# Performance work log

Measured on AMD Instinct MI355X. Metric: run time of the kernel, lower is better.

The kernel has to match this reference:

```python
import jax, jax.numpy as jnp
import numpy as np

EPS = 0.0  # init eps

def setup_inputs() -> dict:
    key = jax.random.key(0)
    k1, k2, k3 = jax.random.split(key, 3)
    n_nodes = 100000
    n_edges = 6400000
    edge_weight = jax.random.uniform(k1, (n_edges,), dtype=jnp.float32)  # non-negative, required by norm='both'
    src = jax.random.randint(k2, (n_edges,), 0, n_nodes, dtype=jnp.int32)
    dst = jax.random.randint(k3, (n_edges,), 0, n_nodes, dtype=jnp.int32)
    return {"edge_weight": edge_weight, "src": src, "dst": dst, "num_nodes": n_nodes}

def reference(edge_weight, src, dst, num_nodes):
    # norm='both': out-degree (weighted) per source node via reversed graph,
    # in-degree (weighted) per destination node; both as segment sums over edges.
    out_deg = jax.ops.segment_sum(edge_weight, src, num_segments=num_nodes) + EPS
    in_deg = jax.ops.segment_sum(edge_weight, dst, num_segments=num_nodes) + EPS
    src_norm = out_deg ** -0.5  # [N]
    dst_norm = in_deg ** -0.5   # [N]
    # gather per-edge norms and multiply with edge weight
    return src_norm[src] * dst_norm[dst] * edge_weight
```

## Files before the change

### kernel.cpp

```cpp
#include <hip/hip_runtime.h>
#include <hip/hip_fp16.h>


#define N_NODES 100000
#define TWO_N   (2 * N_NODES)
#define THREADS 1024
#define GBLK    1024
#define KMAX    4
#define SCALE_F   512.0f
#define INV_SCALE 0.001953125f

__global__ __launch_bounds__(THREADS, 4)
void hist_kernel(const float4* __restrict__ w4,
                 const int4* __restrict__ src4,
                 const int4* __restrict__ dst4,
                 const float* __restrict__ w,
                 const int* __restrict__ src,
                 const int* __restrict__ dst,
                 unsigned* __restrict__ parts,
                 int n4, int n_edges, int P, int C, int bins, int chunk4,
                 int swz)
{
    extern __shared__ unsigned lds[];
    int j, c;
    if (swz) {
        const int x = blockIdx.x & 7;
        const int r = blockIdx.x >> 3;
        j = r % P;
        c = x + 8 * (r / P);
    } else {
        j = blockIdx.x / C;
        c = blockIdx.x - j * C;
    }
    const int lo = j * bins;

    for (int k = threadIdx.x; k < bins; k += THREADS) lds[k] = 0;
    __syncthreads();

    const int beg = c * chunk4;
    const int end = min(n4, beg + chunk4);
    const int t   = threadIdx.x;

#define QUAD(wv, sv, dv)                                                      \
    do {                                                                      \
        unsigned v0 = (unsigned)((wv).x * SCALE_F + 0.5f);                    \
        unsigned v1 = (unsigned)((wv).y * SCALE_F + 0.5f);                    \
        unsigned v2 = (unsigned)((wv).z * SCALE_F + 0.5f);                    \
        unsigned v3 = (unsigned)((wv).w * SCALE_F + 0.5f);                    \
        int a0 = (sv).x - lo, a1 = (sv).y - lo, a2 = (sv).z - lo, a3 = (sv).w - lo; \
        int b0 = (dv).x - lo, b1 = (dv).y - lo, b2 = (dv).z - lo, b3 = (dv).w - lo; \
        if ((unsigned)a0 < (unsigned)bins) atomicAdd(&lds[a0], v0);           \
        if ((unsigned)a1 < (unsigned)bins) atomicAdd(&lds[a1], v1);           \
        if ((unsigned)a2 < (unsigned)bins) atomicAdd(&lds[a2], v2);           \
        if ((unsigned)a3 < (unsigned)bins) atomicAdd(&lds[a3], v3);           \
        if ((unsigned)b0 < (unsigned)bins) atomicAdd(&lds[b0], v0 << 16);     \
        if ((unsigned)b1 < (unsigned)bins) atomicAdd(&lds[b1], v1 << 16);     \
        if ((unsigned)b2 < (unsigned)bins) atomicAdd(&lds[b2], v2 << 16);     \
        if ((unsigned)b3 < (unsigned)bins) atomicAdd(&lds[b3], v3 << 16);     \
    } while (0)

    {
        const int total = end - beg;
        const int trips = (total + 2 * THREADS - 1) / (2 * THREADS);
        int i = beg + t;

        float4 wc0, wc1, wn0, wn1;
        int4   sc0, sc1, sn0, sn1, dc0, dc1, dn0, dn1;
        bool   pc0, pc1, pn0, pn1;

        pn0 = i < end;
        pn1 = (i + THREADS) < end;
        if (pn0) { wn0 = w4[i];           sn0 = src4[i];           dn0 = dst4[i]; }
        if (pn1) { wn1 = w4[i + THREADS]; sn1 = src4[i + THREADS]; dn1 = dst4[i + THREADS]; }

        for (int tr = 0; tr < trips; ++tr) {
            wc0 = wn0; sc0 = sn0; dc0 = dn0; pc0 = pn0;
            wc1 = wn1; sc1 = sn1; dc1 = dn1; pc1 = pn1;

            const int ni = i + 2 * THREADS;
            pn0 = (tr + 1 < trips) && (ni < end);
            pn1 = (tr + 1 < trips) && ((ni + THREADS) < end);
            if (pn0) { wn0 = w4[ni];           sn0 = src4[ni];           dn0 = dst4[ni]; }
            if (pn1) { wn1 = w4[ni + THREADS]; sn1 = src4[ni + THREADS]; dn1 = dst4[ni + THREADS]; }

            __builtin_amdgcn_sched_barrier(0);

            if (pc0) QUAD(wc0, sc0, dc0);
            if (pc1) QUAD(wc1, sc1, dc1);
            i = ni;
        }
    }
#undef QUAD

    if (c == C - 1 && threadIdx.x == 0) {
        for (int e = n4 * 4; e < n_edges; ++e) {
            unsigned v = (unsigned)(w[e] * SCALE_F + 0.5f);
            int a = src[e] - lo;
            int b = dst[e] - lo;
            if ((unsigned)a < (unsigned)bins) atomicAdd(&lds[a], v);
            if ((unsigned)b < (unsigned)bins) atomicAdd(&lds[b], v << 16);
        }
    }

    __syncthreads();
    unsigned* op = parts + ((size_t)j * C + c) * bins;
    for (int k = threadIdx.x; k < bins; k += THREADS)
        __builtin_nontemporal_store(lds[k], op + k);
}

__global__ void reduce_rsqrt_kernel(const unsigned* __restrict__ parts,
                                    __half* __restrict__ normh,
                                    int P, int C, int bins)
{
    int i = blockIdx.x * blockDim.x + threadIdx.x;
    if (i >= N_NODES) return;
    int p = i / bins;
    int b = i - p * bins;
    const unsigned* base = parts + ((size_t)p * C) * bins + b;
    unsigned lo0 = 0, hi0 = 0, lo1 = 0, hi1 = 0, lo2 = 0, hi2 = 0, lo3 = 0, hi3 = 0;
    int c = 0;
    for (; c + 3 < C; c += 4) {
        unsigned v0 = base[(size_t)(c + 0) * bins];
        unsigned v1 = base[(size_t)(c + 1) * bins];
        unsigned v2 = base[(size_t)(c + 2) * bins];
        unsigned v3 = base[(size_t)(c + 3) * bins];
        lo0 += v0 & 0xFFFFu; hi0 += v0 >> 16;
        lo1 += v1 & 0xFFFFu; hi1 += v1 >> 16;
        lo2 += v2 & 0xFFFFu; hi2 += v2 >> 16;
        lo3 += v3 & 0xFFFFu; hi3 += v3 >> 16;
    }
    for (; c < C; ++c) {
        unsigned v = base[(size_t)c * bins];
        lo0 += v & 0xFFFFu; hi0 += v >> 16;
    }
    unsigned lo_s = lo0 + lo1 + lo2 + lo3;
    unsigned hi_s = hi0 + hi1 + hi2 + hi3;
    normh[i]           = __float2half(1.0f / sqrtf((float)lo_s * INV_SCALE));
    normh[N_NODES + i] = __float2half(1.0f / sqrtf((float)hi_s * INV_SCALE));
}

__global__ void degree_atomic_kernel(const float* __restrict__ w,
                                     const int* __restrict__ src,
                                     const int* __restrict__ dst,
                                     float* __restrict__ deg,
                                     int n_edges)
{
    int i = blockIdx.x * blockDim.x + threadIdx.x;
    int stride = gridDim.x * blockDim.x;
    for (; i < n_edges; i += stride) {
        float wi = w[i];
        atomicAdd(&deg[src[i]], wi);
        atomicAdd(&deg[N_NODES + dst[i]], wi);
    }
}

__global__ void rsqrt_half_kernel(const float* __restrict__ deg,
                                  __half* __restrict__ normh, int n)
{
    int i = blockIdx.x * blockDim.x + threadIdx.x;
    if (i < n) normh[i] = __float2half(1.0f / sqrtf(deg[i]));
}

__global__ __launch_bounds__(GBLK, 8)
void prod_kernel(const float4* __restrict__ w4,
                 const int4* __restrict__ src4,
                 const int4* __restrict__ dst4,
                 const __half* __restrict__ srcn_h,
                 const __half* __restrict__ dstn_h,
                 float4* __restrict__ out4,
                 int n4, int n_edges, int qpb, int NR,
                 const float* __restrict__ w,
                 const int* __restrict__ src,
                 const int* __restrict__ dst,
                 float* __restrict__ out)
{
    extern __shared__ __half lh[];
    const int q0   = blockIdx.x * qpb;
    const int qend = min(n4, q0 + qpb);
    const int t    = threadIdx.x;
    const int passes  = (N_NODES + NR - 1) / NR;
    const int half_u4 = NR >> 3;
    const int tot_u4  = NR >> 2;

    float4 pr[KMAX];
    int4   sv[KMAX], dv[KMAX];
    bool   val[KMAX];
#pragma unroll
    for (int k = 0; k < KMAX; ++k) {
        const int q = q0 + k * GBLK + t;
        val[k] = q < qend;
        if (val[k]) {
            pr[k] = w4[q];
            sv[k] = src4[q];
            dv[k] = dst4[q];
        }
    }

    for (int p = 0; p < passes; ++p) {
        if (p > 0) __syncthreads();
        {
            const int base_ = p * NR;
            const uint4* gs = (const uint4*)(srcn_h + base_);
            const uint4* gd = (const uint4*)(dstn_h + base_);
            uint4* lb = (uint4*)lh;
            for (int idx = t; idx < tot_u4; idx += GBLK)
                lb[idx] = (idx < half_u4) ? gs[idx] : gd[idx - half_u4];
        }
        __syncthreads();

        const int lo = p * NR;
        const unsigned lenU = (unsigned)min(NR, N_NODES - lo);
        const __half* ls  = lh;
        const __half* ldt = lh + NR;
#pragma unroll
        for (int k = 0; k < KMAX; ++k) {
            if (!val[k]) continue;
            unsigned a;
            a = (unsigned)(sv[k].x - lo); if (a < lenU) pr[k].x *= __half2float(ls[a]);
            a = (unsigned)(sv[k].y - lo); if (a < lenU) pr[k].y *= __half2float(ls[a]);
            a = (unsigned)(sv[k].z - lo); if (a < lenU) pr[k].z *= __half2float(ls[a]);
            a = (unsigned)(sv[k].w - lo); if (a < lenU) pr[k].w *= __half2float(ls[a]);
            a = (unsigned)(dv[k].x - lo); if (a < lenU) pr[k].x *= __half2float(ldt[a]);
            a = (unsigned)(dv[k].y - lo); if (a < lenU) pr[k].y *= __half2float(ldt[a]);
            a = (unsigned)(dv[k].z - lo); if (a < lenU) pr[k].z *= __half2float(ldt[a]);
            a = (unsigned)(dv[k].w - lo); if (a < lenU) pr[k].w *= __half2float(ldt[a]);
        }
    }

#pragma unroll
    for (int k = 0; k < KMAX; ++k) {
        const int q = q0 + k * GBLK + t;
        if (val[k]) out4[q] = pr[k];
    }

    if (blockIdx.x == 0 && t == 0) {
        for (int e = n4 * 4; e < n_edges; ++e)
            out[e] = __half2float(srcn_h[src[e]]) * __half2float(dstn_h[dst[e]]) * w[e];
    }
}

extern "C" void kernel_launch(void* const* d_in, const int* in_sizes, int n_in,
                              void* d_out, int out_size, void* d_ws, size_t ws_size,
                              hipStream_t stream)
{
    const float* w   = (const float*)d_in[0];
    const int*   src = (const int*)d_in[1];
    const int*   dst = (const int*)d_in[2];
    const int E  = in_sizes[0];
    const int n4 = E >> 2;
    float* out = (float*)d_out;

    __half* normh = (__half*)d_ws;
    char* scratch = (char*)d_ws + (1 << 20);
    unsigned* parts = (unsigned*)scratch;
    float* degf = (float*)scratch;
    size_t avail_u = (ws_size > (1u << 20)) ? (ws_size - (1 << 20)) / 4 : 0;

    const int cands[3] = {163840, 131072, 81920};
    int lds_hist = 65536;
    for (int tC = 0; tC < 3; ++tC)
        if (hipFuncSetAttribute((const void*)hist_kernel,
                                hipFuncAttributeMaxDynamicSharedMemorySize,
                                cands[tC]) == hipSuccess) { lds_hist = cands[tC]; break; }
    int lds_prod = 65536;
    if (hipFuncSetAttribute((const void*)prod_kernel,
                            hipFuncAttributeMaxDynamicSharedMemorySize,
                            81920) == hipSuccess)
        lds_prod = 81920;

    const int bins = lds_hist / 4;
    const int P = (N_NODES + bins - 1) / bins;

    const int blk_per_cu = 163840 / lds_hist;
    int C = (256 * blk_per_cu) / P;
    const size_t per_chunk_u = (size_t)P * (size_t)bins;
    if (avail_u < per_chunk_u) C = 0;
    else {
        int cmax = (int)(avail_u / per_chunk_u);
        if (C > cmax) C = cmax;
    }

    int swz = 0;
    if (C >= 8) { C &= ~7; swz = 1; }

    if (C >= 1) {
        const int chunk4 = (n4 + C - 1) / C;
        hist_kernel<<<P * C, THREADS, (size_t)lds_hist, stream>>>(
            (const float4*)w, (const int4*)src, (const int4*)dst,
            w, src, dst, parts, n4, E, P, C, bins, chunk4, swz);
        reduce_rsqrt_kernel<<<(N_NODES + 255) / 256, 256, 0, stream>>>(
            parts, normh, P, C, bins);
    } else {
        hipMemsetAsync(degf, 0, (size_t)TWO_N * sizeof(float), stream);
        degree_atomic_kernel<<<2048, 256, 0, stream>>>(w, src, dst, degf, E);
        rsqrt_half_kernel<<<(TWO_N + 255) / 256, 256, 0, stream>>>(degf, normh, TWO_N);
    }

    {
        const int NR = lds_prod / 4;
        const int maxq = KMAX * GBLK;
        int C2 = (n4 + maxq - 1) / maxq;
        if (C2 < 512) C2 = 512;
        const int qpb = (n4 + C2 - 1) / C2;
        prod_kernel<<<C2, GBLK, (size_t)lds_prod, stream>>>(
            (const float4*)w, (const int4*)src, (const int4*)dst,
            normh, normh + N_NODES, (float4*)out,
            n4, E, qpb, NR, w, src, dst, out);
    }
}
```

Measured before the change: 68.76 us.

## Pack three 10-bit degree counters per LDS word to cut histogram passes

Histogram counters are repacked from two 16-bit src/dst halves into three 10-bit node counters per 32-bit word, with separate src and dst LDS regions. Each block now covers 1.5x more nodes, which reduces the number of node partitions and so the number of full passes over the edge arrays. The reduce kernel unpacks three fields per word. The cost is coarser weight quantization (1/32) and extra per-atomic index arithmetic, with overflow safety relying on small per-chunk counts.

```diff
diff --git a/kernel.cpp b/kernel.cpp
--- a/kernel.cpp
+++ b/kernel.cpp
@@ -7,8 +7,8 @@
 #define THREADS 1024
 #define GBLK    1024
 #define KMAX    4
-#define SCALE_F   512.0f
-#define INV_SCALE 0.001953125f
+#define SCALE10     32.0f
+#define INV_SCALE10 0.03125f
 
 __global__ __launch_bounds__(THREADS, 4)
 void hist_kernel(const float4* __restrict__ w4,
@@ -18,7 +18,7 @@
                  const int* __restrict__ src,
                  const int* __restrict__ dst,
                  unsigned* __restrict__ parts,
-                 int n4, int n_edges, int P, int C, int bins, int chunk4,
+                 int n4, int n_edges, int P, int C, int binw, int chunk4,
                  int swz)
 {
     extern __shared__ unsigned lds[];
@@ -32,31 +32,39 @@
         j = blockIdx.x / C;
         c = blockIdx.x - j * C;
     }
-    const int lo = j * bins;
-
-    for (int k = threadIdx.x; k < bins; k += THREADS) lds[k] = 0;
+    const int NRH = 3 * binw;
+    const int lo  = j * NRH;
+    const unsigned ubinw = (unsigned)binw;
+    const unsigned uNRH  = (unsigned)NRH;
+    unsigned* __restrict__ ldsd = lds + binw;
+
+    for (int k = threadIdx.x; k < 2 * binw; k += THREADS) lds[k] = 0;
     __syncthreads();
 
     const int beg = c * chunk4;
     const int end = min(n4, beg + chunk4);
     const int t   = threadIdx.x;
 
+#define ENDP(nd, vq, base_)                                                   \
+    do {                                                                      \
+        unsigned l_ = (unsigned)((nd) - lo);                                  \
+        if (l_ < uNRH) {                                                      \
+            unsigned f_ = (unsigned)(l_ >= ubinw) + (unsigned)(l_ >= 2u * ubinw); \
+            unsigned wd_ = l_ - f_ * ubinw;                                   \
+            atomicAdd(&base_[wd_], (vq) << (10u * f_));                       \
+        }                                                                     \
+    } while (0)
+
 #define QUAD(wv, sv, dv)                                                      \
     do {                                                                      \
-        unsigned v0 = (unsigned)((wv).x * SCALE_F + 0.5f);                    \
-        unsigned v1 = (unsigned)((wv).y * SCALE_F + 0.5f);                    \
-        unsigned v2 = (unsigned)((wv).z * SCALE_F + 0.5f);                    \
-        unsigned v3 = (unsigned)((wv).w * SCALE_F + 0.5f);                    \
-        int a0 = (sv).x - lo, a1 = (sv).y - lo, a2 = (sv).z - lo, a3 = (sv).w - lo; \
-        int b0 = (dv).x - lo, b1 = (dv).y - lo, b2 = (dv).z - lo, b3 = (dv).w - lo; \
-        if ((unsigned)a0 < (unsigned)bins) atomicAdd(&lds[a0], v0);           \
-        if ((unsigned)a1 < (unsigned)bins) atomicAdd(&lds[a1], v1);           \
-        if ((unsigned)a2 < (unsigned)bins) atomicAdd(&lds[a2], v2);           \
-        if ((unsigned)a3 < (unsigned)bins) atomicAdd(&lds[a3], v3);           \
-        if ((unsigned)b0 < (unsigned)bins) atomicAdd(&lds[b0], v0 << 16);     \
-        if ((unsigned)b1 < (unsigned)bins) atomicAdd(&lds[b1], v1 << 16);     \
-        if ((unsigned)b2 < (unsigned)bins) atomicAdd(&lds[b2], v2 << 16);     \
-        if ((unsigned)b3 < (unsigned)bins) atomicAdd(&lds[b3], v3 << 16);     \
+        unsigned v0 = (unsigned)((wv).x * SCALE10 + 0.5f);                    \
+        unsigned v1 = (unsigned)((wv).y * SCALE10 + 0.5f);                    \
+        unsigned v2 = (unsigned)((wv).z * SCALE10 + 0.5f);                    \
+        unsigned v3 = (unsigned)((wv).w * SCALE10 + 0.5f);                    \
+        ENDP((sv).x, v0, lds);  ENDP((sv).y, v1, lds);                        \
+        ENDP((sv).z, v2, lds);  ENDP((sv).w, v3, lds);                        \
+        ENDP((dv).x, v0, ldsd); ENDP((dv).y, v1, ldsd);                       \
+        ENDP((dv).z, v2, ldsd); ENDP((dv).w, v3, ldsd);                       \
     } while (0)
 
     {
@@ -94,49 +102,55 @@
 
     if (c == C - 1 && threadIdx.x == 0) {
         for (int e = n4 * 4; e < n_edges; ++e) {
-            unsigned v = (unsigned)(w[e] * SCALE_F + 0.5f);
-            int a = src[e] - lo;
-            int b = dst[e] - lo;
-            if ((unsigned)a < (unsigned)bins) atomicAdd(&lds[a], v);
-            if ((unsigned)b < (unsigned)bins) atomicAdd(&lds[b], v << 16);
-        }
-    }
+            unsigned v = (unsigned)(w[e] * SCALE10 + 0.5f);
+            ENDP(src[e], v, lds);
+            ENDP(dst[e], v, ldsd);
+        }
+    }
+#undef ENDP
 
     __syncthreads();
-    unsigned* op = parts + ((size_t)j * C + c) * bins;
-    for (int k = threadIdx.x; k < bins; k += THREADS)
+    unsigned* op = parts + (size_t)(j * C + c) * (2 * binw);
+    for (int k = threadIdx.x; k < 2 * binw; k += THREADS)
         __builtin_nontemporal_store(lds[k], op + k);
 }
 
 __global__ void reduce_rsqrt_kernel(const unsigned* __restrict__ parts,
                                     __half* __restrict__ normh,
-                                    int P, int C, int bins)
-{
-    int i = blockIdx.x * blockDim.x + threadIdx.x;
-    if (i >= N_NODES) return;
-    int p = i / bins;
-    int b = i - p * bins;
-    const unsigned* base = parts + ((size_t)p * C) * bins + b;
-    unsigned lo0 = 0, hi0 = 0, lo1 = 0, hi1 = 0, lo2 = 0, hi2 = 0, lo3 = 0, hi3 = 0;
-    int c = 0;
-    for (; c + 3 < C; c += 4) {
-        unsigned v0 = base[(size_t)(c + 0) * bins];
-        unsigned v1 = base[(size_t)(c + 1) * bins];
-        unsigned v2 = base[(size_t)(c + 2) * bins];
-        unsigned v3 = base[(size_t)(c + 3) * bins];
-        lo0 += v0 & 0xFFFFu; hi0 += v0 >> 16;
-        lo1 += v1 & 0xFFFFu; hi1 += v1 >> 16;
-        lo2 += v2 & 0xFFFFu; hi2 += v2 >> 16;
-        lo3 += v3 & 0xFFFFu; hi3 += v3 >> 16;
-    }
-    for (; c < C; ++c) {
-        unsigned v = base[(size_t)c * bins];
-        lo0 += v & 0xFFFFu; hi0 += v >> 16;
-    }
-    unsigned lo_s = lo0 + lo1 + lo2 + lo3;
-    unsigned hi_s = hi0 + hi1 + hi2 + hi3;
-    normh[i]           = __float2half(1.0f / sqrtf((float)lo_s * INV_SCALE));
-    normh[N_NODES + i] = __float2half(1.0f / sqrtf((float)hi_s * INV_SCALE));
+                                    int P, int C, int binw)
+{
+    const int tid = blockIdx.x * blockDim.x + threadIdx.x;
+    if (tid >= P * binw) return;
+    const int j  = tid / binw;
+    const int wd = tid - j * binw;
+    const int NRH = 3 * binw;
+    const size_t stride = (size_t)2 * binw;
+    const unsigned* base = parts + (size_t)j * C * stride + wd;
+
+    unsigned s0 = 0, s1 = 0, s2 = 0, d0 = 0, d1 = 0, d2 = 0;
+#pragma unroll 4
+    for (int c = 0; c < C; ++c) {
+        const unsigned vs = base[(size_t)c * stride];
+        const unsigned vd = base[(size_t)c * stride + binw];
+        s0 += vs & 1023u; s1 += (vs >> 10) & 1023u; s2 += (vs >> 20) & 1023u;
+        d0 += vd & 1023u; d1 += (vd >> 10) & 1023u; d2 += (vd >> 20) & 1023u;
+    }
+
+    const int n0 = j * NRH + wd;
+    const int n1 = n0 + binw;
+    const int n2 = n0 + 2 * binw;
+    if (n0 < N_NODES) {
+        normh[n0]           = __float2half(1.0f / sqrtf((float)s0 * INV_SCALE10));
+        normh[N_NODES + n0] = __float2half(1.0f / sqrtf((float)d0 * INV_SCALE10));
+    }
+    if (n1 < N_NODES) {
+        normh[n1]           = __float2half(1.0f / sqrtf((float)s1 * INV_SCALE10));
+        normh[N_NODES + n1] = __float2half(1.0f / sqrtf((float)d1 * INV_SCALE10));
+    }
+    if (n2 < N_NODES) {
+        normh[n2]           = __float2half(1.0f / sqrtf((float)s2 * INV_SCALE10));
+        normh[N_NODES + n2] = __float2half(1.0f / sqrtf((float)d2 * INV_SCALE10));
+    }
 }
 
 __global__ void degree_atomic_kernel(const float* __restrict__ w,
@@ -268,12 +282,13 @@
                             81920) == hipSuccess)
         lds_prod = 81920;
 
-    const int bins = lds_hist / 4;
-    const int P = (N_NODES + bins - 1) / bins;
+    const int binw = lds_hist / 8;
+    const int NRH  = 3 * binw;
+    const int P = (N_NODES + NRH - 1) / NRH;
 
     const int blk_per_cu = 163840 / lds_hist;
     int C = (256 * blk_per_cu) / P;
-    const size_t per_chunk_u = (size_t)P * (size_t)bins;
+    const size_t per_chunk_u = (size_t)P * (size_t)(2 * binw);
     if (avail_u < per_chunk_u) C = 0;
     else {
         int cmax = (int)(avail_u / per_chunk_u);
@@ -287,9 +302,10 @@
         const int chunk4 = (n4 + C - 1) / C;
         hist_kernel<<<P * C, THREADS, (size_t)lds_hist, stream>>>(
             (const float4*)w, (const int4*)src, (const int4*)dst,
-            w, src, dst, parts, n4, E, P, C, bins, chunk4, swz);
-        reduce_rsqrt_kernel<<<(N_NODES + 255) / 256, 256, 0, stream>>>(
-            parts, normh, P, C, bins);
+            w, src, dst, parts, n4, E, P, C, binw, chunk4, swz);
+        const int rthreads = P * binw;
+        reduce_rsqrt_kernel<<<(rthreads + 255) / 256, 256, 0, stream>>>(
+            parts, normh, P, C, binw);
     } else {
         hipMemsetAsync(degf, 0, (size_t)TWO_N * sizeof(float), stream);
         degree_atomic_kernel<<<2048, 256, 0, stream>>>(w, src, dst, degf, E);
```

Result: slower. 77.06 us (+12.1%).
